# Optimization experiments

Measured on AMD Instinct MI355X. Metric: run time of the kernel, lower is better.

The kernel has to match this reference:

```python
import jax, jax.numpy as jnp
import numpy as np

N = 4096          # particles
BOX_LEN = 10.0    # cubic box edge
CUTOFF = 0.5
SKIN = 0.1        # kept for parity with module; fresh build uses cutoff+skin then filters to cutoff


def setup_inputs() -> dict:
    key = jax.random.key(0)
    positions = jax.random.uniform(key, (N, 3), dtype=jnp.float32) * BOX_LEN
    box_vectors = jnp.diag(jnp.full((3,), BOX_LEN, dtype=jnp.float32))
    i_np, j_np = np.triu_indices(N, k=1)  # all unique pairs i<j, P = N(N-1)/2
    return {
        "positions": positions,
        "box_vectors": box_vectors,
        "i_pairs": jnp.asarray(i_np, dtype=jnp.int32),
        "j_pairs": jnp.asarray(j_np, dtype=jnp.int32),
    }


def reference(positions, box_vectors, i_pairs, j_pairs):
    # Displacement with periodic boundary conditions (orthorhombic box).
    box_lengths = jnp.diagonal(box_vectors)            # [3]
    half = box_lengths * 0.5
    r_ij = positions[i_pairs] - positions[j_pairs]     # [P,3] gather + subtract
    r_ij = jnp.remainder(r_ij + half, box_lengths) - half
    d_ij = jnp.linalg.norm(r_ij, axis=1, keepdims=True)  # [P,1]

    # cutoff filter; jit-compatible compaction expressed as masking
    mask = (d_ij <= CUTOFF)[:, 0]                      # [P]
    r_m = jnp.where(mask[:, None], r_ij, 0.0)
    d_m = jnp.where(mask[:, None], d_ij, 0.0)

    # symmetric doubling (only_unique_pairs=False branch): (i,j) and (j,i)
    pairs = jnp.stack([
        jnp.concatenate([i_pairs, j_pairs]),
        jnp.concatenate([j_pairs, i_pairs]),
    ]).astype(jnp.int64)                               # [2, 2P]
    r_full = jnp.concatenate([r_m, -r_m], axis=0)      # [2P,3]
    d_full = jnp.concatenate([d_m, d_m], axis=0)       # [2P,1]
    mask_full = jnp.concatenate([mask, mask])          # [2P] valid-pair mask
    return pairs, d_full, r_full, mask_full
```

## Files before the change

### kernel.cpp

```cpp
#include <hip/hip_runtime.h>
#include <math.h>


#define CUTOFF_F 0.5f

__device__ __forceinline__ float pbc_wrap(float r, float L, float h) {
    float t = __fadd_rn(r, h);
    float m = fmodf(t, L);
    if (m < 0.0f) m = __fadd_rn(m, L);
    return __fsub_rn(m, h);
}

__global__ __launch_bounds__(256)
void nl_nsq_kernel(const float* __restrict__ pos,
                   const float* __restrict__ box,
                   const int*   __restrict__ ip,
                   const int*   __restrict__ jp,
                   float*       __restrict__ out,
                   long long P) {
    long long p = (long long)blockIdx.x * blockDim.x + threadIdx.x;
    if (p >= P) return;

    const int i = ip[p];
    const int j = jp[p];

    const float Lx = box[0], Ly = box[4], Lz = box[8];
    const float hx = Lx * 0.5f, hy = Ly * 0.5f, hz = Lz * 0.5f;

    float rx = __fsub_rn(pos[3 * i + 0], pos[3 * j + 0]);
    float ry = __fsub_rn(pos[3 * i + 1], pos[3 * j + 1]);
    float rz = __fsub_rn(pos[3 * i + 2], pos[3 * j + 2]);

    rx = pbc_wrap(rx, Lx, hx);
    ry = pbc_wrap(ry, Ly, hy);
    rz = pbc_wrap(rz, Lz, hz);

    float d2 = __fadd_rn(__fadd_rn(__fmul_rn(rx, rx), __fmul_rn(ry, ry)),
                         __fmul_rn(rz, rz));
    float d = sqrtf(d2);

    const bool keep = (d <= CUTOFF_F);
    const float dm  = keep ? d  : 0.0f;
    const float mx  = keep ? rx : 0.0f;
    const float my  = keep ? ry : 0.0f;
    const float mz  = keep ? rz : 0.0f;
    const float mk  = keep ? 1.0f : 0.0f;

    const float fi = (float)i;
    const float fj = (float)j;

    out[p]          = fi;
    out[P + p]      = fj;
    out[2 * P + p]  = fj;
    out[3 * P + p]  = fi;
    out[4 * P + p]  = dm;
    out[5 * P + p]  = dm;
    {
        long long b0 = 6 * P + 3 * p;
        out[b0 + 0] = mx;
        out[b0 + 1] = my;
        out[b0 + 2] = mz;
        long long b1 = 6 * P + 3 * (P + p);
        out[b1 + 0] = -mx;
        out[b1 + 1] = -my;
        out[b1 + 2] = -mz;
    }
    out[12 * P + p] = mk;
    out[13 * P + p] = mk;
}

extern "C" void kernel_launch(void* const* d_in, const int* in_sizes, int n_in,
                              void* d_out, int out_size, void* d_ws, size_t ws_size,
                              hipStream_t stream) {
    const float* pos = (const float*)d_in[0];
    const float* box = (const float*)d_in[1];
    const int*   ip  = (const int*)d_in[2];
    const int*   jp  = (const int*)d_in[3];
    float*       out = (float*)d_out;

    const long long P = (long long)in_sizes[2];

    const int block = 256;
    const long long grid = (P + block - 1) / block;
    nl_nsq_kernel<<<(dim3)(unsigned)grid, block, 0, stream>>>(pos, box, ip, jp, out, P);
}
```

Baseline: 499.6 us.

## Stage displacement vectors in LDS for vectorized nontemporal stores, replace fmodf wrap

Each thread now processes four pairs per block. The interleaved xyz displacement output is staged through shared memory so it can be written with coalesced float4 nontemporal stores for both the positive and negated copies. Scalar outputs also use nontemporal stores. The fmodf periodic wrap is replaced by a single conditional add or subtract, which is valid only when displacements lie within one box length, as they do for in-box positions. The changes target the stride-3 uncoalesced stores and the cost of fmodf, in exchange for a __syncthreads, LDS use and a separate tail path.

```diff
diff --git a/kernel.cpp b/kernel.cpp
--- a/kernel.cpp
+++ b/kernel.cpp
@@ -3,70 +3,129 @@
 
 
 #define CUTOFF_F 0.5f
+#define BLOCK 256
+#define SPT 4
+#define PPB (BLOCK * SPT)
 
-__device__ __forceinline__ float pbc_wrap(float r, float L, float h) {
+typedef float fx4 __attribute__((ext_vector_type(4)));
+
+__device__ __forceinline__ float pbc_wrap_fast(float r, float L, float h) {
     float t = __fadd_rn(r, h);
-    float m = fmodf(t, L);
-    if (m < 0.0f) m = __fadd_rn(m, L);
+    float m = (t >= L) ? __fsub_rn(t, L)
+            : (t < 0.0f ? __fadd_rn(t, L)
+                        : t);
     return __fsub_rn(m, h);
 }
 
-__global__ __launch_bounds__(256)
+__device__ __forceinline__ void compute_pair(const float* __restrict__ pos,
+                                             float Lx, float Ly, float Lz,
+                                             float hx, float hy, float hz,
+                                             int i, int j,
+                                             float& fi, float& fj, float& dm,
+                                             float& mx, float& my, float& mz,
+                                             float& mk) {
+    float rx = __fsub_rn(pos[3 * i + 0], pos[3 * j + 0]);
+    float ry = __fsub_rn(pos[3 * i + 1], pos[3 * j + 1]);
+    float rz = __fsub_rn(pos[3 * i + 2], pos[3 * j + 2]);
+
+    rx = pbc_wrap_fast(rx, Lx, hx);
+    ry = pbc_wrap_fast(ry, Ly, hy);
+    rz = pbc_wrap_fast(rz, Lz, hz);
+
+    float d2 = __fadd_rn(__fadd_rn(__fmul_rn(rx, rx), __fmul_rn(ry, ry)),
+                         __fmul_rn(rz, rz));
+    float d = sqrtf(d2);
+
+    const bool keep = (d <= CUTOFF_F);
+    dm = keep ? d  : 0.0f;
+    mx = keep ? rx : 0.0f;
+    my = keep ? ry : 0.0f;
+    mz = keep ? rz : 0.0f;
+    mk = keep ? 1.0f : 0.0f;
+    fi = (float)i;
+    fj = (float)j;
+}
+
+__device__ __forceinline__ void nt_store(float* p, float v) {
+    __builtin_nontemporal_store(v, p);
+}
+__device__ __forceinline__ void nt_store4(float* p, fx4 v) {
+    __builtin_nontemporal_store(v, (fx4*)p);
+}
+
+__global__ __launch_bounds__(BLOCK)
 void nl_nsq_kernel(const float* __restrict__ pos,
                    const float* __restrict__ box,
                    const int*   __restrict__ ip,
                    const int*   __restrict__ jp,
                    float*       __restrict__ out,
                    long long P) {
-    long long p = (long long)blockIdx.x * blockDim.x + threadIdx.x;
-    if (p >= P) return;
+    __shared__ float lds_r[PPB * 3];
 
-    const int i = ip[p];
-    const int j = jp[p];
+    const int t = threadIdx.x;
+    const long long base = (long long)blockIdx.x * PPB;
 
     const float Lx = box[0], Ly = box[4], Lz = box[8];
     const float hx = Lx * 0.5f, hy = Ly * 0.5f, hz = Lz * 0.5f;
 
-    float rx = __fsub_rn(pos[3 * i + 0], pos[3 * j + 0]);
-    float ry = __fsub_rn(pos[3 * i + 1], pos[3 * j + 1]);
-    float rz = __fsub_rn(pos[3 * i + 2], pos[3 * j + 2]);
+    if (base + PPB <= P) {
+#pragma unroll
+        for (int s = 0; s < SPT; ++s) {
+            const int  lp = t + s * BLOCK;
+            const long long p = base + lp;
+            const int i = ip[p];
+            const int j = jp[p];
 
-    rx = pbc_wrap(rx, Lx, hx);
-    ry = pbc_wrap(ry, Ly, hy);
-    rz = pbc_wrap(rz, Lz, hz);
+            float fi, fj, dm, mx, my, mz, mk;
+            compute_pair(pos, Lx, Ly, Lz, hx, hy, hz, i, j,
+                         fi, fj, dm, mx, my, mz, mk);
 
-    float d2 = __fadd_rn(__fadd_rn(__fmul_rn(rx, rx), __fmul_rn(ry, ry)),
-                         __fmul_rn(rz, rz));
-    float d = sqrtf(d2);
+            nt_store(&out[p],          fi);
+            nt_store(&out[P + p],      fj);
+            nt_store(&out[2 * P + p],  fj);
+            nt_store(&out[3 * P + p],  fi);
+            nt_store(&out[4 * P + p],  dm);
+            nt_store(&out[5 * P + p],  dm);
+            nt_store(&out[12 * P + p], mk);
+            nt_store(&out[13 * P + p], mk);
 
-    const bool keep = (d <= CUTOFF_F);
-    const float dm  = keep ? d  : 0.0f;
-    const float mx  = keep ? rx : 0.0f;
-    const float my  = keep ? ry : 0.0f;
-    const float mz  = keep ? rz : 0.0f;
-    const float mk  = keep ? 1.0f : 0.0f;
+            lds_r[3 * lp + 0] = mx;
+            lds_r[3 * lp + 1] = my;
+            lds_r[3 * lp + 2] = mz;
+        }
 
-    const float fi = (float)i;
-    const float fj = (float)j;
+        __syncthreads();
 
-    out[p]          = fi;
-    out[P + p]      = fj;
-    out[2 * P + p]  = fj;
-    out[3 * P + p]  = fi;
-    out[4 * P + p]  = dm;
-    out[5 * P + p]  = dm;
-    {
-        long long b0 = 6 * P + 3 * p;
-        out[b0 + 0] = mx;
-        out[b0 + 1] = my;
-        out[b0 + 2] = mz;
-        long long b1 = 6 * P + 3 * (P + p);
-        out[b1 + 0] = -mx;
-        out[b1 + 1] = -my;
-        out[b1 + 2] = -mz;
+        const fx4* lr = (const fx4*)lds_r;
+        const long long rpos = 6 * P;
+        const long long rneg = 9 * P;
+        const long long boff = (long long)blockIdx.x * (PPB * 3);
+#pragma unroll
+        for (int s = 0; s < 3; ++s) {
+            const int idx = t + s * BLOCK;
+            const fx4 v = lr[idx];
+            nt_store4(&out[rpos + boff + 4 * idx], v);
+            nt_store4(&out[rneg + boff + 4 * idx], -v);
+        }
+    } else {
+        for (long long p = base + t; p < P; p += BLOCK) {
+            float fi, fj, dm, mx, my, mz, mk;
+            compute_pair(pos, Lx, Ly, Lz, hx, hy, hz, ip[p], jp[p],
+                         fi, fj, dm, mx, my, mz, mk);
+            out[p]          = fi;
+            out[P + p]      = fj;
+            out[2 * P + p]  = fj;
+            out[3 * P + p]  = fi;
+            out[4 * P + p]  = dm;
+            out[5 * P + p]  = dm;
+            long long b0 = 6 * P + 3 * p;
+            out[b0 + 0] = mx;  out[b0 + 1] = my;  out[b0 + 2] = mz;
+            long long b1 = 6 * P + 3 * (P + p);
+            out[b1 + 0] = -mx; out[b1 + 1] = -my; out[b1 + 2] = -mz;
+            out[12 * P + p] = mk;
+            out[13 * P + p] = mk;
+        }
     }
-    out[12 * P + p] = mk;
-    out[13 * P + p] = mk;
 }
 
 extern "C" void kernel_launch(void* const* d_in, const int* in_sizes, int n_in,
@@ -79,8 +138,7 @@
     float*       out = (float*)d_out;
 
     const long long P = (long long)in_sizes[2];
+    const long long grid = (P + PPB - 1) / PPB;
 
-    const int block = 256;
-    const long long grid = (P + block - 1) / block;
-    nl_nsq_kernel<<<(dim3)(unsigned)grid, block, 0, stream>>>(pos, box, ip, jp, out, P);
+    nl_nsq_kernel<<<(dim3)(unsigned)grid, BLOCK, 0, stream>>>(pos, box, ip, jp, out, P);
 }
```

Result: slower. 512.8 us (+2.6%).
